# Performance work log

Hardware: AMD Instinct MI355X
Metric: run time of the kernel (lower is better)

## Reference

```python
import jax, jax.numpy as jnp
import numpy as np

M_FACTORS = [8, 8, 8, 8]
N_FACTORS = [8, 8, 8, 8]
RANK = 8
E = 8
B = 8
SEQ = 512
M_IN = int(np.prod(M_FACTORS))   # 4096
N_OUT = int(np.prod(N_FACTORS))  # 4096


def setup_inputs() -> dict:
    key = jax.random.key(0)
    k1, k2, k3, k4, k5 = jax.random.split(key, 5)
    X = jax.random.normal(k1, (B, SEQ, M_IN), dtype=jnp.float32)
    gates = jax.random.uniform(k2, (B, E), dtype=jnp.float32)
    # TT cores: [E, r_i, factor, r_{i+1}]; boundary ranks are 1.
    core_first = jax.random.normal(k3, (E, 1, M_FACTORS[0], RANK), dtype=jnp.float32)
    cores_mid = jax.random.normal(k4, (6, E, RANK, 8, RANK), dtype=jnp.float32)
    core_last = jax.random.normal(k5, (E, RANK, N_FACTORS[-1], 1), dtype=jnp.float32)
    return {"X": X, "gates": gates, "core_first": core_first,
            "cores_mid": cores_mid, "core_last": core_last}


def _tt_forward(X, gates, core_first, cores_mid, core_last):
    b, s, _ = X.shape
    # View X as [B, 1, seq, m_k-1, ..., m_0] (m factors reversed), rank dim = 1.
    tt = X.reshape((b, s) + tuple(M_FACTORS[::-1]))[:, None]
    cores = [core_first] + [cores_mid[i] for i in range(cores_mid.shape[0])] + [core_last]
    num_m = len(M_FACTORS)
    # Input-factor contractions: 'b r ... m, b r m p -> b p ...'
    for i in range(num_m):
        merged = jnp.einsum('be,ermp->brmp', gates, cores[i])  # [B, r, m_f, p]
        tt = jnp.einsum('br...m,brmp->bp...', tt, merged)
    # Output-factor expansions: 'b r ..., b r n p -> b p ... n'
    for i in range(len(N_FACTORS)):
        merged = jnp.einsum('be,ernp->brnp', gates, cores[num_m + i])  # [B, r, n_f, p]
        tt = jnp.einsum('br...,brnp->bp...n', tt, merged)
    return tt.reshape(b, s, -1)  # [B, seq, prod(n_factors)]


def reference(X, gates, core_first, cores_mid, core_last):
    return _tt_forward(X, gates, core_first, cores_mid, core_last)
```

## Files before the change

### kernel.cpp

```cpp
#include <hip/hip_runtime.h>

typedef float f32x4 __attribute__((ext_vector_type(4)));

#define GLOBAL_AS __attribute__((address_space(1)))
#define SHARED_AS __attribute__((address_space(3)))


__global__ __launch_bounds__(256) void k_compose(
    const float* __restrict__ gates,
    const float* __restrict__ core_first,
    const float* __restrict__ cores_mid,
    const float* __restrict__ core_last,
    float* __restrict__ KinT,
    float* __restrict__ Kout)
{
  const int part = blockIdx.x;
  const int b    = blockIdx.y;
  const int t    = threadIdx.x;

  __shared__ float g[8];
  __shared__ float mg[3200];
  __shared__ __align__(16) float A2[512];
  __shared__ __align__(16) float A3[512 * 9];
  __shared__ __align__(16) float C2[512];
  __shared__ __align__(16) float C3[4096];

  if (t < 8) g[t] = gates[b*8 + t];
  __syncthreads();

  for (int idx = t; idx < 3200; idx += 256) {
    float acc = 0.f;
    if (idx < 64) {
      #pragma unroll
      for (int e = 0; e < 8; ++e) acc += g[e] * core_first[e*64 + idx];
    } else if (idx < 3136) {
      const int i = (idx - 64) >> 9;
      const int w = (idx - 64) & 511;
      #pragma unroll
      for (int e = 0; e < 8; ++e) acc += g[e] * cores_mid[(i*8 + e)*512 + w];
    } else {
      const int w = idx - 3136;
      #pragma unroll
      for (int e = 0; e < 8; ++e) acc += g[e] * core_last[e*64 + w];
    }
    mg[idx] = acc;
  }
  __syncthreads();

  const float* mg0 = mg;
  const float* mg1 = mg + 64;
  const float* mg2 = mg + 64 + 512;
  const float* mg3 = mg + 64 + 1024;
  const float* mg4 = mg + 64 + 1536;
  const float* mg5 = mg + 64 + 2048;
  const float* mg6 = mg + 64 + 2560;
  const float* mg7 = mg + 3136;

  for (int idx = t; idx < 1024; idx += 256) {
    if (idx < 512) {
      const int mm = idx >> 3, p2 = idx & 7;
      const int m1 = mm >> 3, m0 = mm & 7;
      float acc = 0.f;
      #pragma unroll
      for (int p1 = 0; p1 < 8; ++p1)
        acc += mg0[m0*8 + p1] * mg1[p1*64 + m1*8 + p2];
      A2[idx] = acc;
    } else {
      const int id = idx - 512;
      const int p6 = id >> 6, n2 = (id >> 3) & 7, n3 = id & 7;
      float acc = 0.f;
      #pragma unroll
      for (int p7 = 0; p7 < 8; ++p7)
        acc += mg6[p6*64 + n2*8 + p7] * mg7[p7*8 + n3];
      C2[id] = acc;
    }
  }
  __syncthreads();

  for (int idx = t; idx < 8192; idx += 256) {
    if (idx < 4096) {
      const int rest = idx >> 3, p3 = idx & 7;
      const int m2 = rest >> 6, mm = rest & 63;
      float acc = 0.f;
      #pragma unroll
      for (int p2 = 0; p2 < 8; ++p2)
        acc += A2[mm*8 + p2] * mg2[p2*64 + m2*8 + p3];
      A3[rest*9 + p3] = acc;
    } else {
      const int id = idx - 4096;
      const int p5 = id >> 9, n1 = (id >> 6) & 7, nn = id & 63;
      float acc = 0.f;
      #pragma unroll
      for (int p6 = 0; p6 < 8; ++p6)
        acc += mg5[p5*64 + n1*8 + p6] * C2[p6*64 + nn];
      C3[id] = acc;
    }
  }
  __syncthreads();

  {
    float* kb = KinT + b*32768;
    #pragma unroll
    for (int rr = 0; rr < 2; ++rr) {
      const int r = rr*256 + t;
      #pragma unroll
      for (int p4 = 0; p4 < 8; ++p4) {
        float acc = 0.f;
        #pragma unroll
        for (int p3 = 0; p3 < 8; ++p3)
          acc += A3[r*9 + p3] * mg3[p3*64 + part*8 + p4];
        kb[p4*4096 + part*512 + r] = acc;
      }
    }
    float* ob = Kout + b*32768 + part*512;
    #pragma unroll
    for (int jj = 0; jj < 2; ++jj) {
      const int j = jj*256 + t;
      #pragma unroll
      for (int p4 = 0; p4 < 8; ++p4) {
        float acc = 0.f;
        #pragma unroll
        for (int p5 = 0; p5 < 8; ++p5)
          acc += mg4[p4*64 + part*8 + p5] * C3[p5*512 + j];
        ob[p4*4096 + j] = acc;
      }
    }
  }
}

__global__ __launch_bounds__(256) void k_fused(
    const float* __restrict__ X,
    const float* __restrict__ KinT,
    const float* __restrict__ Kout,
    float* __restrict__ Out)
{
  const int stile = blockIdx.x;
  const int b     = blockIdx.y;
  const int t     = threadIdx.x;
  const int lane  = t & 63;
  const int w     = t >> 6;

  __shared__ __align__(16) float xb[2][8 * 512];
  __shared__ __align__(16) float kb[2][8 * 512];
  __shared__ float vs[8 * 8];

  const int s0 = stile * 8;
  const float* xsrc = X    + ((size_t)(b*512 + s0)) * 4096;
  const float* ksrc = KinT + (size_t)b*32768;

#define STAGE(c, u) do {                                                      \
    const int coff_ = (c)*512;                                                \
    _Pragma("unroll")                                                         \
    for (int i_ = 0; i_ < 4; ++i_) {                                          \
      const int s_    = w + i_*4;                                  \
      const int row_  = s_ >> 1;                           \
      const int half_ = (s_ & 1) * 256;                                       \
      const float* gx_ = xsrc + (size_t)row_*4096 + coff_ + half_ + lane*4;   \
      const float* gk_ = ksrc + (size_t)row_*4096 + coff_ + half_ + lane*4;   \
      __builtin_amdgcn_global_load_lds(                                       \
          (const GLOBAL_AS void*)gx_,                                         \
          (SHARED_AS void*)&xb[u][row_*512 + half_], 16, 0, 0);               \
      __builtin_amdgcn_global_load_lds(                                       \
          (const GLOBAL_AS void*)gk_,                                         \
          (SHARED_AS void*)&kb[u][row_*512 + half_], 16, 0, 0);               \
    }                                                                         \
  } while (0)

  const int r0 = w*2, r1 = w*2 + 1;

  f32x4 acc0[8], acc1[8];
  #pragma unroll
  for (int p = 0; p < 8; ++p) { acc0[p] = (f32x4)0.f; acc1[p] = (f32x4)0.f; }

  STAGE(0, 0);
  __syncthreads();

  #pragma unroll
  for (int c = 0; c < 8; ++c) {
    const int u = c & 1;
    if (c < 7) STAGE(c + 1, u ^ 1);

    #pragma unroll
    for (int g = 0; g < 2; ++g) {
      const f32x4 x0 = *(const f32x4*)&xb[u][r0*512 + g*256 + lane*4];
      const f32x4 x1 = *(const f32x4*)&xb[u][r1*512 + g*256 + lane*4];
      #pragma unroll
      for (int p = 0; p < 8; ++p) {
        const f32x4 k = *(const f32x4*)&kb[u][p*512 + g*256 + lane*4];
        acc0[p] += x0 * k;
        acc1[p] += x1 * k;
      }
    }
    __syncthreads();
  }
#undef STAGE

  #pragma unroll
  for (int p = 0; p < 8; ++p) {
    float s0v = acc0[p].x + acc0[p].y + acc0[p].z + acc0[p].w;
    float s1v = acc1[p].x + acc1[p].y + acc1[p].z + acc1[p].w;
    #pragma unroll
    for (int d = 1; d < 64; d <<= 1) {
      s0v += __shfl_xor(s0v, d);
      s1v += __shfl_xor(s1v, d);
    }
    if (lane == 0) {
      vs[r0*8 + p] = s0v;
      vs[r1*8 + p] = s1v;
    }
  }
  __syncthreads();

  float4 vA[8], vB[8];
  #pragma unroll
  for (int s = 0; s < 8; ++s) {
    vA[s] = *(const float4*)(vs + s*8);
    vB[s] = *(const float4*)(vs + s*8 + 4);
  }

  const float* kob = Kout + (size_t)b*32768 + t*4;
  float*       ob  = Out + ((size_t)(b*512 + s0))*4096 + t*4;

  #pragma unroll
  for (int nc = 0; nc < 4; ++nc) {
    float4 kr[8];
    #pragma unroll
    for (int p = 0; p < 8; ++p)
      kr[p] = *(const float4*)(kob + p*4096 + nc*1024);
    #pragma unroll
    for (int s = 0; s < 8; ++s) {
      f32x4 o;
      o.x = vA[s].x*kr[0].x + vA[s].y*kr[1].x + vA[s].z*kr[2].x + vA[s].w*kr[3].x
          + vB[s].x*kr[4].x + vB[s].y*kr[5].x + vB[s].z*kr[6].x + vB[s].w*kr[7].x;
      o.y = vA[s].x*kr[0].y + vA[s].y*kr[1].y + vA[s].z*kr[2].y + vA[s].w*kr[3].y
          + vB[s].x*kr[4].y + vB[s].y*kr[5].y + vB[s].z*kr[6].y + vB[s].w*kr[7].y;
      o.z = vA[s].x*kr[0].z + vA[s].y*kr[1].z + vA[s].z*kr[2].z + vA[s].w*kr[3].z
          + vB[s].x*kr[4].z + vB[s].y*kr[5].z + vB[s].z*kr[6].z + vB[s].w*kr[7].z;
      o.w = vA[s].x*kr[0].w + vA[s].y*kr[1].w + vA[s].z*kr[2].w + vA[s].w*kr[3].w
          + vB[s].x*kr[4].w + vB[s].y*kr[5].w + vB[s].z*kr[6].w + vB[s].w*kr[7].w;
      __builtin_nontemporal_store(o, (f32x4*)(ob + (size_t)s*4096 + nc*1024));
    }
  }
}

extern "C" void kernel_launch(void* const* d_in, const int* in_sizes, int n_in,
                              void* d_out, int out_size, void* d_ws, size_t ws_size,
                              hipStream_t stream) {
  const float* X     = (const float*)d_in[0];
  const float* gates = (const float*)d_in[1];
  const float* cf    = (const float*)d_in[2];
  const float* cm    = (const float*)d_in[3];
  const float* cl    = (const float*)d_in[4];
  float* out = (float*)d_out;

  float* ws   = (float*)d_ws;
  float* KinT = ws;
  float* Kout = ws + 262144;

  k_compose<<<dim3(8, 8),  256, 0, stream>>>(gates, cf, cm, cl, KinT, Kout);
  k_fused <<<dim3(64, 8), 256, 0, stream>>>(X, KinT, Kout, out);
}
```

Baseline: 169.4 us.

## Split compose kernel across z-blocks and deepen fused kernel load pipeline

The compose kernel now launches 8x more blocks. Each block computes only a quarter of either the input-side or the output-side factor chain, which cuts per-block serial work and shared memory. The fused kernel replaces its double-buffered 512-wide chunks with a 4-stage ring of 256-wide chunks. It uses explicit vmcnt waits and raw barriers so three chunks of loads are in flight at once. The compose split duplicates some merged-core computation across blocks, and the manual waitcnt scheme depends on the exact count of outstanding loads.

After: 159.8 us. -5.7%, faster.

```diff
diff --git a/kernel.cpp b/kernel.cpp
--- a/kernel.cpp
+++ b/kernel.cpp
@@ -16,114 +16,123 @@
 {
   const int part = blockIdx.x;
   const int b    = blockIdx.y;
+  const int z    = blockIdx.z;
   const int t    = threadIdx.x;
 
   __shared__ float g[8];
-  __shared__ float mg[3200];
-  __shared__ __align__(16) float A2[512];
-  __shared__ __align__(16) float A3[512 * 9];
-  __shared__ __align__(16) float C2[512];
-  __shared__ __align__(16) float C3[4096];
+  __shared__ float mg[1600];
+  __shared__ __align__(16) float S1[512];
+  __shared__ __align__(16) float S2[128 * 9];
 
   if (t < 8) g[t] = gates[b*8 + t];
   __syncthreads();
 
-  for (int idx = t; idx < 3200; idx += 256) {
-    float acc = 0.f;
-    if (idx < 64) {
-      #pragma unroll
-      for (int e = 0; e < 8; ++e) acc += g[e] * core_first[e*64 + idx];
-    } else if (idx < 3136) {
-      const int i = (idx - 64) >> 9;
-      const int w = (idx - 64) & 511;
-      #pragma unroll
-      for (int e = 0; e < 8; ++e) acc += g[e] * cores_mid[(i*8 + e)*512 + w];
-    } else {
-      const int w = idx - 3136;
-      #pragma unroll
-      for (int e = 0; e < 8; ++e) acc += g[e] * core_last[e*64 + w];
-    }
-    mg[idx] = acc;
-  }
-  __syncthreads();
-
-  const float* mg0 = mg;
-  const float* mg1 = mg + 64;
-  const float* mg2 = mg + 64 + 512;
-  const float* mg3 = mg + 64 + 1024;
-  const float* mg4 = mg + 64 + 1536;
-  const float* mg5 = mg + 64 + 2048;
-  const float* mg6 = mg + 64 + 2560;
-  const float* mg7 = mg + 3136;
-
-  for (int idx = t; idx < 1024; idx += 256) {
-    if (idx < 512) {
+  if (z < 4) {
+    for (int idx = t; idx < 1600; idx += 256) {
+      float acc = 0.f;
+      if (idx < 64) {
+        #pragma unroll
+        for (int e = 0; e < 8; ++e) acc += g[e] * core_first[e*64 + idx];
+      } else {
+        const int i = (idx - 64) >> 9;
+        const int w2 = (idx - 64) & 511;
+        #pragma unroll
+        for (int e = 0; e < 8; ++e) acc += g[e] * cores_mid[(i*8 + e)*512 + w2];
+      }
+      mg[idx] = acc;
+    }
+    __syncthreads();
+
+    #pragma unroll
+    for (int i = 0; i < 2; ++i) {
+      const int idx = i*256 + t;
       const int mm = idx >> 3, p2 = idx & 7;
       const int m1 = mm >> 3, m0 = mm & 7;
       float acc = 0.f;
       #pragma unroll
       for (int p1 = 0; p1 < 8; ++p1)
-        acc += mg0[m0*8 + p1] * mg1[p1*64 + m1*8 + p2];
-      A2[idx] = acc;
-    } else {
-      const int id = idx - 512;
+        acc += mg[m0*8 + p1] * mg[64 + p1*64 + m1*8 + p2];
+      S1[idx] = acc;
+    }
+    __syncthreads();
+
+    #pragma unroll
+    for (int i = 0; i < 4; ++i) {
+      const int idx = i*256 + t;
+      const int rl = idx >> 3, p3 = idx & 7;
+      const int m2 = 2*z + (rl >> 6), mm = rl & 63;
+      float acc = 0.f;
+      #pragma unroll
+      for (int p2 = 0; p2 < 8; ++p2)
+        acc += S1[mm*8 + p2] * mg[576 + p2*64 + m2*8 + p3];
+      S2[rl*9 + p3] = acc;
+    }
+    __syncthreads();
+
+    float* kb = KinT + b*32768;
+    #pragma unroll
+    for (int i = 0; i < 4; ++i) {
+      const int idx = i*256 + t;
+      const int rl = idx >> 3, p4 = idx & 7;
+      float acc = 0.f;
+      #pragma unroll
+      for (int p3 = 0; p3 < 8; ++p3)
+        acc += S2[rl*9 + p3] * mg[1088 + p3*64 + part*8 + p4];
+      kb[p4*4096 + part*512 + z*128 + rl] = acc;
+    }
+  } else {
+    const int zz = z - 4;
+    for (int idx = t; idx < 1600; idx += 256) {
+      float acc = 0.f;
+      if (idx < 1536) {
+        const int i = 3 + (idx >> 9);
+        const int w2 = idx & 511;
+        #pragma unroll
+        for (int e = 0; e < 8; ++e) acc += g[e] * cores_mid[(i*8 + e)*512 + w2];
+      } else {
+        const int w2 = idx - 1536;
+        #pragma unroll
+        for (int e = 0; e < 8; ++e) acc += g[e] * core_last[e*64 + w2];
+      }
+      mg[idx] = acc;
+    }
+    __syncthreads();
+
+    #pragma unroll
+    for (int i = 0; i < 2; ++i) {
+      const int id = i*256 + t;
       const int p6 = id >> 6, n2 = (id >> 3) & 7, n3 = id & 7;
       float acc = 0.f;
       #pragma unroll
       for (int p7 = 0; p7 < 8; ++p7)
-        acc += mg6[p6*64 + n2*8 + p7] * mg7[p7*8 + n3];
-      C2[id] = acc;
-    }
-  }
-  __syncthreads();
-
-  for (int idx = t; idx < 8192; idx += 256) {
-    if (idx < 4096) {
-      const int rest = idx >> 3, p3 = idx & 7;
-      const int m2 = rest >> 6, mm = rest & 63;
-      float acc = 0.f;
-      #pragma unroll
-      for (int p2 = 0; p2 < 8; ++p2)
-        acc += A2[mm*8 + p2] * mg2[p2*64 + m2*8 + p3];
-      A3[rest*9 + p3] = acc;
-    } else {
-      const int id = idx - 4096;
-      const int p5 = id >> 9, n1 = (id >> 6) & 7, nn = id & 63;
+        acc += mg[1024 + p6*64 + n2*8 + p7] * mg[1536 + p7*8 + n3];
+      S1[id] = acc;
+    }
+    __syncthreads();
+
+    #pragma unroll
+    for (int i = 0; i < 4; ++i) {
+      const int idx = i*256 + t;
+      const int p5 = idx >> 7, jl = idx & 127;
+      const int n1 = 2*zz + (jl >> 6), nn = jl & 63;
       float acc = 0.f;
       #pragma unroll
       for (int p6 = 0; p6 < 8; ++p6)
-        acc += mg5[p5*64 + n1*8 + p6] * C2[p6*64 + nn];
-      C3[id] = acc;
-    }
-  }
-  __syncthreads();
-
-  {
-    float* kb = KinT + b*32768;
-    #pragma unroll
-    for (int rr = 0; rr < 2; ++rr) {
-      const int r = rr*256 + t;
-      #pragma unroll
-      for (int p4 = 0; p4 < 8; ++p4) {
-        float acc = 0.f;
-        #pragma unroll
-        for (int p3 = 0; p3 < 8; ++p3)
-          acc += A3[r*9 + p3] * mg3[p3*64 + part*8 + p4];
-        kb[p4*4096 + part*512 + r] = acc;
-      }
-    }
-    float* ob = Kout + b*32768 + part*512;
-    #pragma unroll
-    for (int jj = 0; jj < 2; ++jj) {
-      const int j = jj*256 + t;
-      #pragma unroll
-      for (int p4 = 0; p4 < 8; ++p4) {
-        float acc = 0.f;
-        #pragma unroll
-        for (int p5 = 0; p5 < 8; ++p5)
-          acc += mg4[p4*64 + part*8 + p5] * C3[p5*512 + j];
-        ob[p4*4096 + j] = acc;
-      }
+        acc += mg[512 + p5*64 + n1*8 + p6] * S1[p6*64 + nn];
+      S2[p5*128 + jl] = acc;
+    }
+    __syncthreads();
+
+    float* ob = Kout + b*32768 + part*512 + zz*128;
+    #pragma unroll
+    for (int i = 0; i < 4; ++i) {
+      const int idx = i*256 + t;
+      const int jl = idx >> 3, p4 = idx & 7;
+      float acc = 0.f;
+      #pragma unroll
+      for (int p5 = 0; p5 < 8; ++p5)
+        acc += mg[p4*64 + part*8 + p5] * S2[p5*128 + jl];
+      ob[p4*4096 + jl] = acc;
     }
   }
 }
@@ -140,30 +149,28 @@
   const int lane  = t & 63;
   const int w     = t >> 6;
 
-  __shared__ __align__(16) float xb[2][8 * 512];
-  __shared__ __align__(16) float kb[2][8 * 512];
+  __shared__ __align__(16) float xs[4][8 * 256];
+  __shared__ __align__(16) float ks[4][8 * 256];
   __shared__ float vs[8 * 8];
 
   const int s0 = stile * 8;
   const float* xsrc = X    + ((size_t)(b*512 + s0)) * 4096;
   const float* ksrc = KinT + (size_t)b*32768;
 
-#define STAGE(c, u) do {                                                      \
-    const int coff_ = (c)*512;                                                \
-    _Pragma("unroll")                                                         \
-    for (int i_ = 0; i_ < 4; ++i_) {                                          \
-      const int s_    = w + i_*4;                                  \
-      const int row_  = s_ >> 1;                           \
-      const int half_ = (s_ & 1) * 256;                                       \
-      const float* gx_ = xsrc + (size_t)row_*4096 + coff_ + half_ + lane*4;   \
-      const float* gk_ = ksrc + (size_t)row_*4096 + coff_ + half_ + lane*4;   \
-      __builtin_amdgcn_global_load_lds(                                       \
-          (const GLOBAL_AS void*)gx_,                                         \
-          (SHARED_AS void*)&xb[u][row_*512 + half_], 16, 0, 0);               \
-      __builtin_amdgcn_global_load_lds(                                       \
-          (const GLOBAL_AS void*)gk_,                                         \
-          (SHARED_AS void*)&kb[u][row_*512 + half_], 16, 0, 0);               \
-    }                                                                         \
+#define STAGE(c, u) do {                                                       \
+    const int off_ = (c)*256 + lane*4;                                         \
+    __builtin_amdgcn_global_load_lds(                                          \
+        (const GLOBAL_AS void*)(xsrc + (size_t)(w)*4096 + off_),               \
+        (SHARED_AS void*)&xs[u][(w)*256], 16, 0, 0);                           \
+    __builtin_amdgcn_global_load_lds(                                          \
+        (const GLOBAL_AS void*)(xsrc + (size_t)(w + 4)*4096 + off_),           \
+        (SHARED_AS void*)&xs[u][(w + 4)*256], 16, 0, 0);                       \
+    __builtin_amdgcn_global_load_lds(                                          \
+        (const GLOBAL_AS void*)(ksrc + (size_t)(w)*4096 + off_),               \
+        (SHARED_AS void*)&ks[u][(w)*256], 16, 0, 0);                           \
+    __builtin_amdgcn_global_load_lds(                                          \
+        (const GLOBAL_AS void*)(ksrc + (size_t)(w + 4)*4096 + off_),           \
+        (SHARED_AS void*)&ks[u][(w + 4)*256], 16, 0, 0);                       \
   } while (0)
 
   const int r0 = w*2, r1 = w*2 + 1;
@@ -173,25 +180,26 @@
   for (int p = 0; p < 8; ++p) { acc0[p] = (f32x4)0.f; acc1[p] = (f32x4)0.f; }
 
   STAGE(0, 0);
-  __syncthreads();
-
-  #pragma unroll
-  for (int c = 0; c < 8; ++c) {
-    const int u = c & 1;
-    if (c < 7) STAGE(c + 1, u ^ 1);
-
-    #pragma unroll
-    for (int g = 0; g < 2; ++g) {
-      const f32x4 x0 = *(const f32x4*)&xb[u][r0*512 + g*256 + lane*4];
-      const f32x4 x1 = *(const f32x4*)&xb[u][r1*512 + g*256 + lane*4];
-      #pragma unroll
-      for (int p = 0; p < 8; ++p) {
-        const f32x4 k = *(const f32x4*)&kb[u][p*512 + g*256 + lane*4];
-        acc0[p] += x0 * k;
-        acc1[p] += x1 * k;
-      }
-    }
-    __syncthreads();
+  STAGE(1, 1);
+  STAGE(2, 2);
+
+  #pragma unroll
+  for (int c = 0; c < 16; ++c) {
+    if (c <= 13)      asm volatile("s_waitcnt vmcnt(8)" ::: "memory");
+    else if (c == 14) asm volatile("s_waitcnt vmcnt(4)" ::: "memory");
+    else              asm volatile("s_waitcnt vmcnt(0)" ::: "memory");
+    __builtin_amdgcn_s_barrier();
+    if (c + 3 < 16) STAGE(c + 3, (c + 3) & 3);
+
+    const int u = c & 3;
+    const f32x4 x0 = *(const f32x4*)&xs[u][r0*256 + lane*4];
+    const f32x4 x1 = *(const f32x4*)&xs[u][r1*256 + lane*4];
+    #pragma unroll
+    for (int p = 0; p < 8; ++p) {
+      const f32x4 k = *(const f32x4*)&ks[u][p*256 + lane*4];
+      acc0[p] += x0 * k;
+      acc1[p] += x1 * k;
+    }
   }
 #undef STAGE
 
@@ -257,6 +265,6 @@
   float* KinT = ws;
   float* Kout = ws + 262144;
 
-  k_compose<<<dim3(8, 8),  256, 0, stream>>>(gates, cf, cm, cl, KinT, Kout);
-  k_fused <<<dim3(64, 8), 256, 0, stream>>>(X, KinT, Kout, out);
+  k_compose<<<dim3(8, 8, 8), 256, 0, stream>>>(gates, cf, cm, cl, KinT, Kout);
+  k_fused  <<<dim3(64, 8),   256, 0, stream>>>(X, KinT, Kout, out);
 }
```
